# Kernel tuning notes

Hardware: AMD Instinct MI355X
Metric: run time of the kernel (lower is better)

## Reference

```python
import jax, jax.numpy as jnp
import numpy as np

HIDDEN = 1024
B, S = 4, 2048

def setup_inputs() -> dict:
    key = jax.random.key(0)
    k1, k2 = jax.random.split(key)
    hidden_states = jax.random.normal(k1, (B, S, HIDDEN), dtype=jnp.float32)
    # torch nn.Linear weight layout: [out_features, in_features]
    W_proj = jax.random.normal(k2, (3 * HIDDEN, HIDDEN), dtype=jnp.float32) * (1.0 / np.sqrt(HIDDEN))
    b_proj = jnp.zeros((3 * HIDDEN,), dtype=jnp.float32)
    return {"hidden_states": hidden_states, "W_proj": W_proj, "b_proj": b_proj}

def reference(hidden_states, W_proj, b_proj):
    h = hidden_states.shape[-1]
    # fused QKV projection: y = x @ W^T + b
    qkv = jnp.einsum('bsh,oh->bso', hidden_states, W_proj) + b_proj
    q, k, v = jnp.split(qkv, 3, axis=-1)  # each [B,S,H]
    scale = 1.0 / jnp.sqrt(jnp.asarray(h, dtype=q.dtype))
    scores = jnp.einsum('bqh,bkh->bqk', q, k) * scale  # [B,S,S]
    attn = jax.nn.softmax(scores, axis=-1)
    out = jnp.einsum('bqk,bkh->bqh', attn, v)
    return out
```

## Files before the change

kernel.cpp:

```cpp
#include <hip/hip_runtime.h>
#include <stdint.h>

#define HIDDEN 1024
#define BATCH  4
#define SEQ    2048
#define TOKENS (BATCH * SEQ)
#define QKVD   (3 * HIDDEN)

typedef unsigned short u16;
typedef __attribute__((ext_vector_type(8))) short   short8;
typedef __attribute__((ext_vector_type(4))) float   floatx4;

__device__ __forceinline__ u16 f32_bf16_rne(float f) {
    unsigned int u = __float_as_uint(f);
    u += 0x7FFFu + ((u >> 16) & 1u);
    return (u16)(u >> 16);
}

__device__ __forceinline__ void gl16(const u16* g, u16* l) {
    __builtin_amdgcn_global_load_lds(
        (const __attribute__((address_space(1))) void*)g,
        (__attribute__((address_space(3))) void*)l, 16, 0, 0);
}

#define SYNC3() do { __builtin_amdgcn_sched_barrier(0); \
    asm volatile("s_waitcnt vmcnt(3)\n\ts_barrier" ::: "memory"); } while (0)
#define PBAR() do { __builtin_amdgcn_sched_barrier(0); \
    asm volatile("s_barrier" ::: "memory"); } while (0)
#define LG0() asm volatile("s_waitcnt lgkmcnt(0)" ::: "memory")
#define VM4() do { __builtin_amdgcn_sched_barrier(0); \
    asm volatile("s_waitcnt vmcnt(4)" ::: "memory"); } while (0)

__global__ __launch_bounds__(256) void cvt2_bf16_kernel(
        const float* __restrict__ sa, const float* __restrict__ sb,
        u16* __restrict__ da, u16* __restrict__ db, int n4a, int n4tot) {
    int i = blockIdx.x * 256 + threadIdx.x;
    if (i >= n4tot) return;
    float4 v;
    if (i < n4a) v = ((const float4*)sa)[i];
    else         v = ((const float4*)sb)[i - n4a];
    ushort4 o;
    o.x = f32_bf16_rne(v.x); o.y = f32_bf16_rne(v.y);
    o.z = f32_bf16_rne(v.z); o.w = f32_bf16_rne(v.w);
    if (i < n4a) ((ushort4*)da)[i] = o;
    else         ((ushort4*)db)[i - n4a] = o;
}

__global__ __launch_bounds__(512, 2) void gemm_qkv(
        const u16* __restrict__ A, const u16* __restrict__ B,
        u16* __restrict__ C, const float* __restrict__ bias) {
    __shared__ __align__(16) u16 lds[2][2][(128 + 256) * 32];

    const int t    = threadIdx.x;
    const int lane = t & 63;
    const int wid  = t >> 6;
    const int wr   = wid >> 2;
    const int wc   = wid & 3;
    const int bm   = blockIdx.y * 128;
    const int bn   = blockIdx.x * 256;

    const int rA  = t >> 2;
    const int sl  = (t & 3) ^ ((rA >> 1) & 3);
    const u16* gA  = A + (size_t)(bm + rA) * 1024 + sl * 8;
    const u16* gB0 = B + (size_t)(bn + rA) * 1024 + sl * 8;
    const u16* gB1 = gB0 + (size_t)128 * 1024;

    const int fr = lane & 15;
    const int kc = lane >> 4;
    const int fo = ((kc ^ ((fr >> 1) & 3)) << 4);
    const int aoffB = (wr * 64 + fr) * 64 + fo;
    const int boffB = (wc * 64 + fr) * 64 + fo;

    floatx4 acc[4][4];
#pragma unroll
    for (int i = 0; i < 4; i++)
#pragma unroll
        for (int j = 0; j < 4; j++) acc[i][j] = (floatx4){0.f, 0.f, 0.f, 0.f};

    short8 bfr0, bfr1, bfr2, bfr3, va0, va1;

#define LDB4(BASE) \
    bfr0 = *(const short8*)((BASE) + boffB);        \
    bfr1 = *(const short8*)((BASE) + boffB + 1024); \
    bfr2 = *(const short8*)((BASE) + boffB + 2048); \
    bfr3 = *(const short8*)((BASE) + boffB + 3072);

#define MFMA2(MI, A0, A1) \
    __builtin_amdgcn_s_setprio(1); \
    acc[MI][0]     = __builtin_amdgcn_mfma_f32_16x16x32_bf16(A0, bfr0, acc[MI][0], 0, 0, 0); \
    acc[MI][1]     = __builtin_amdgcn_mfma_f32_16x16x32_bf16(A0, bfr1, acc[MI][1], 0, 0, 0); \
    acc[MI][2]     = __builtin_amdgcn_mfma_f32_16x16x32_bf16(A0, bfr2, acc[MI][2], 0, 0, 0); \
    acc[MI][3]     = __builtin_amdgcn_mfma_f32_16x16x32_bf16(A0, bfr3, acc[MI][3], 0, 0, 0); \
    acc[(MI)+1][0] = __builtin_amdgcn_mfma_f32_16x16x32_bf16(A1, bfr0, acc[(MI)+1][0], 0, 0, 0); \
    acc[(MI)+1][1] = __builtin_amdgcn_mfma_f32_16x16x32_bf16(A1, bfr1, acc[(MI)+1][1], 0, 0, 0); \
    acc[(MI)+1][2] = __builtin_amdgcn_mfma_f32_16x16x32_bf16(A1, bfr2, acc[(MI)+1][2], 0, 0, 0); \
    acc[(MI)+1][3] = __builtin_amdgcn_mfma_f32_16x16x32_bf16(A1, bfr3, acc[(MI)+1][3], 0, 0, 0); \
    __builtin_amdgcn_s_setprio(0);

#define ITER(BUF, SBUF, SCOL) { \
    const char* As0_ = (const char*)&lds[BUF][0][0]; \
    const char* Bs0_ = As0_ + 8192; \
    const char* As1_ = (const char*)&lds[BUF][1][0]; \
    const char* Bs1_ = As1_ + 8192; \
    gl16(gA + (SCOL),       (u16*)((char*)&lds[SBUF][0][0]    + wid * 1024)); \
    LDB4(Bs0_); \
    va0 = *(const short8*)(As0_ + aoffB); \
    va1 = *(const short8*)(As0_ + aoffB + 1024); \
    MFMA2(0, va0, va1); \
    gl16(gB0 + (SCOL),      (u16*)((char*)&lds[SBUF][0][4096] + wid * 1024)); \
    gl16(gB1 + (SCOL),      (u16*)((char*)&lds[SBUF][0][8192] + wid * 1024)); \
    va0 = *(const short8*)(As0_ + aoffB + 2048); \
    va1 = *(const short8*)(As0_ + aoffB + 3072); \
    MFMA2(2, va0, va1); \
    SYNC3(); \
    gl16(gA + (SCOL) + 32,  (u16*)((char*)&lds[SBUF][1][0]    + wid * 1024)); \
    LDB4(Bs1_); \
    va0 = *(const short8*)(As1_ + aoffB); \
    va1 = *(const short8*)(As1_ + aoffB + 1024); \
    MFMA2(0, va0, va1); \
    gl16(gB0 + (SCOL) + 32, (u16*)((char*)&lds[SBUF][1][4096] + wid * 1024)); \
    gl16(gB1 + (SCOL) + 32, (u16*)((char*)&lds[SBUF][1][8192] + wid * 1024)); \
    va0 = *(const short8*)(As1_ + aoffB + 2048); \
    va1 = *(const short8*)(As1_ + aoffB + 3072); \
    MFMA2(2, va0, va1); \
    SYNC3(); }

    gl16(gA,       (u16*)((char*)&lds[0][0][0]    + wid * 1024));
    gl16(gB0,      (u16*)((char*)&lds[0][0][4096] + wid * 1024));
    gl16(gB1,      (u16*)((char*)&lds[0][0][8192] + wid * 1024));
    gl16(gA + 32,  (u16*)((char*)&lds[0][1][0]    + wid * 1024));
    gl16(gB0 + 32, (u16*)((char*)&lds[0][1][4096] + wid * 1024));
    gl16(gB1 + 32, (u16*)((char*)&lds[0][1][8192] + wid * 1024));
    SYNC3();

    const int nk = 1024 >> 6;
    for (int kt = 0; kt < nk; kt += 2) {
        const int c1 = (kt + 1) << 6;
        const int c2 = (kt + 2 < nk ? (kt + 2) : (nk - 1)) << 6;
        ITER(0, 1, c1)
        ITER(1, 0, c2)
    }
    asm volatile("s_waitcnt vmcnt(0)" ::: "memory");

#undef ITER
#undef MFMA2
#undef LDB4

    const int crow0 = bm + wr * 64 + kc * 4;
    const int ccol0 = bn + wc * 64 + fr;
    float bv[4];
#pragma unroll
    for (int ni = 0; ni < 4; ni++) bv[ni] = bias[ccol0 + ni * 16];
#pragma unroll
    for (int mi = 0; mi < 4; mi++)
#pragma unroll
        for (int ni = 0; ni < 4; ni++)
#pragma unroll
            for (int r = 0; r < 4; r++)
                C[(size_t)(crow0 + mi * 16 + r) * QKVD + (ccol0 + ni * 16)] =
                    f32_bf16_rne(acc[mi][ni][r] + bv[ni]);
}

template <int EPI, int WM>
__global__ __launch_bounds__(512, 2) void gemm_bt(
        const u16* __restrict__ A, const u16* __restrict__ B,
        void* __restrict__ Cv, const float* __restrict__ bias,
        int K, int lda, int ldb, int ldc,
        size_t sA, size_t sB, size_t sC, float scale) {
    constexpr int BM    = 2 * WM;
    constexpr int MIH   = WM / 32;
    constexpr int ASLAB = BM * 64;
    constexpr int BSLAB = 256 * 64;
    constexpr int BUFB  = 2 * ASLAB + 2 * BSLAB;
    __shared__ __align__(16) char lds[2][BUFB];

    const int t    = threadIdx.x;
    const int lane = t & 63;
    const int wid  = t >> 6;
    const int wr   = wid >> 2;
    const int wc   = wid & 3;
    const int bm   = blockIdx.y * BM;
    const int bn   = blockIdx.x * 256;

    const u16* Ab = A + (size_t)blockIdx.z * sA;
    const u16* Bb = B + (size_t)blockIdx.z * sB;

    const int r0 = t >> 2;
    const int sl = (t & 3) ^ ((r0 >> 1) & 3);
    const u16* gA0 = Ab + (size_t)(bm + r0) * lda + sl * 8;
    const u16* gA1 = gA0 + (size_t)128 * lda;
    const u16* gB0 = Bb + (size_t)(bn + r0) * ldb + sl * 8;
    const u16* gB1 = gB0 + (size_t)128 * ldb;

    const int fr  = lane & 15;
    const int kc  = lane >> 4;
    const int frb = fr * 64 + ((kc ^ ((fr >> 1) & 3)) << 4);

    floatx4 acc[2 * MIH][4];
#pragma unroll
    for (int i = 0; i < 2 * MIH; i++)
#pragma unroll
        for (int j = 0; j < 4; j++) acc[i][j] = (floatx4){0.f, 0.f, 0.f, 0.f};

    short8 aF[MIH][2], bLo[2][2], bHi[2][2];

    auto rdA = [&](short8 (&dst)[MIH][2], const char* bp, int miBase) {
#pragma unroll
        for (int m = 0; m < MIH; m++)
#pragma unroll
            for (int ks = 0; ks < 2; ks++)
                dst[m][ks] = *(const short8*)(bp + ks * ASLAB +
                    (wr * WM + (miBase + m) * 16) * 64 + frb);
    };
    auto rdB = [&](short8 (&dst)[2][2], const char* bp, int niBase) {
#pragma unroll
        for (int n = 0; n < 2; n++)
#pragma unroll
            for (int ks = 0; ks < 2; ks++)
                dst[n][ks] = *(const short8*)(bp + 2 * ASLAB + ks * BSLAB +
                    (wc * 64 + (niBase + n) * 16) * 64 + frb);
    };
    auto mf = [&](short8 (&av)[MIH][2], short8 (&bv)[2][2], int miB, int niB) {
        __builtin_amdgcn_s_setprio(1);
#pragma unroll
        for (int m = 0; m < MIH; m++)
#pragma unroll
            for (int n = 0; n < 2; n++)
#pragma unroll
                for (int ks = 0; ks < 2; ks++)
                    acc[miB + m][niB + n] = __builtin_amdgcn_mfma_f32_16x16x32_bf16(
                        av[m][ks], bv[n][ks], acc[miB + m][niB + n], 0, 0, 0);
        __builtin_amdgcn_s_setprio(0);
    };

#define STA(buf, ks, sc) do { \
    char* d = &lds[buf][(ks) * ASLAB] + wid * 1024; \
    gl16(gA0 + (sc) + (ks) * 32, (u16*)d); \
    if constexpr (WM == 128) gl16(gA1 + (sc) + (ks) * 32, (u16*)(d + 8192)); \
  } while (0)
#define STB(buf, ks, sc) do { \
    char* d = &lds[buf][2 * ASLAB + (ks) * BSLAB] + wid * 1024; \
    gl16(gB0 + (sc) + (ks) * 32, (u16*)d); \
    gl16(gB1 + (sc) + (ks) * 32, (u16*)(d + 8192)); \
  } while (0)

#define GROUP(q, S1, S2, S3, S4) { \
    const char* bp = &lds[q][0]; \
    rdA(aF, bp, 0); rdB(bLo, bp, 0); S1; PBAR(); LG0(); \
    mf(aF, bLo, 0, 0);   PBAR(); \
    rdB(bHi, bp, 2);                S2; PBAR(); LG0(); \
    mf(aF, bHi, 0, 2);   PBAR(); \
    rdA(aF, bp, MIH);               S3; PBAR(); LG0(); \
    mf(aF, bHi, MIH, 2); PBAR(); \
    S4; VM4(); PBAR(); \
    mf(aF, bLo, MIH, 0); PBAR(); \
}

    STA(0, 0, 0); STA(0, 1, 0); STB(0, 0, 0); STB(0, 1, 0);
    STB(1, 0, 64); STB(1, 1, 64);
    VM4(); PBAR();

    const int nk = K >> 6;
    for (int T = 0; T < nk; T += 2) {
        const int c1 = (T + 1) << 6;
        const int c2 = (T + 2 < nk ? T + 2 : nk - 1) << 6;
        const int c3 = (T + 3 < nk ? T + 3 : nk - 1) << 6;
        GROUP(0, STA(1, 0, c1), STA(1, 1, c1), STB(0, 0, c2), STB(0, 1, c2))
        GROUP(1, STA(0, 0, c2), STA(0, 1, c2), STB(1, 0, c3), STB(1, 1, c3))
    }
    asm volatile("s_waitcnt vmcnt(0)" ::: "memory");

#undef GROUP
#undef STB
#undef STA

    const int crow0 = bm + wr * WM + kc * 4;
    const int ccol0 = bn + wc * 64 + fr;
    const size_t coff = (size_t)blockIdx.z * sC;

    float* C = (float*)Cv;
#pragma unroll
    for (int mi = 0; mi < 2 * MIH; mi++)
#pragma unroll
        for (int ni = 0; ni < 4; ni++)
#pragma unroll
            for (int r = 0; r < 4; r++) {
                float v = acc[mi][ni][r];
                if (EPI == 1) v *= scale;
                C[coff + (size_t)(crow0 + mi * 16 + r) * ldc + (ccol0 + ni * 16)] = v;
            }
}

__global__ __launch_bounds__(256) void softmax_tr_kernel(
        const float* __restrict__ S, u16* __restrict__ P,
        const u16* __restrict__ qkv, u16* __restrict__ Vt) {
    __shared__ float redm[4];
    __shared__ float reds[4];
    __shared__ u16 tile[64][66];
    const int t = threadIdx.x;

    if ((int)blockIdx.x < TOKENS) {
        const size_t base = (size_t)blockIdx.x * SEQ;
        const int lane = t & 63, wid = t >> 6;
        const float4* src = (const float4*)(S + base);
        float4 a = src[t], b = src[t + 256];

        float m = fmaxf(fmaxf(fmaxf(a.x, a.y), fmaxf(a.z, a.w)),
                        fmaxf(fmaxf(b.x, b.y), fmaxf(b.z, b.w)));
#pragma unroll
        for (int off = 32; off; off >>= 1) m = fmaxf(m, __shfl_xor(m, off, 64));
        if (lane == 0) redm[wid] = m;
        __syncthreads();
        m = fmaxf(fmaxf(redm[0], redm[1]), fmaxf(redm[2], redm[3]));

        float e[8];
        e[0] = __expf(a.x - m); e[1] = __expf(a.y - m);
        e[2] = __expf(a.z - m); e[3] = __expf(a.w - m);
        e[4] = __expf(b.x - m); e[5] = __expf(b.y - m);
        e[6] = __expf(b.z - m); e[7] = __expf(b.w - m);
        float s = e[0] + e[1] + e[2] + e[3] + e[4] + e[5] + e[6] + e[7];
#pragma unroll
        for (int off = 32; off; off >>= 1) s += __shfl_xor(s, off, 64);
        if (lane == 0) reds[wid] = s;
        __syncthreads();
        s = reds[0] + reds[1] + reds[2] + reds[3];
        const float r = 1.f / s;

        ushort4* dst = (ushort4*)(P + base);
        ushort4 o0, o1;
        o0.x = f32_bf16_rne(e[0] * r); o0.y = f32_bf16_rne(e[1] * r);
        o0.z = f32_bf16_rne(e[2] * r); o0.w = f32_bf16_rne(e[3] * r);
        o1.x = f32_bf16_rne(e[4] * r); o1.y = f32_bf16_rne(e[5] * r);
        o1.z = f32_bf16_rne(e[6] * r); o1.w = f32_bf16_rne(e[7] * r);
        dst[t] = o0;
        dst[t + 256] = o1;
    } else {
        const int bx = blockIdx.x - TOKENS;
        const int b  = bx >> 9;
        const int s0 = (bx & 31) * 64;
        const int h0 = ((bx >> 5) & 15) * 64;
        const int c = t & 63, r4 = t >> 6;
#pragma unroll
        for (int i = 0; i < 16; i++) {
            int sl = i * 4 + r4;
            tile[sl][c] = qkv[(size_t)(b * SEQ + s0 + sl) * QKVD + 2 * HIDDEN + h0 + c];
        }
        __syncthreads();
#pragma unroll
        for (int i = 0; i < 16; i++) {
            int hl = i * 4 + r4;
            Vt[(size_t)(b * HIDDEN + h0 + hl) * SEQ + s0 + c] = tile[c][hl];
        }
    }
}

extern "C" void kernel_launch(void* const* d_in, const int* in_sizes, int n_in,
                              void* d_out, int out_size, void* d_ws, size_t ws_size,
                              hipStream_t stream) {
    const float* x    = (const float*)d_in[0];
    const float* W    = (const float*)d_in[1];
    const float* bias = (const float*)d_in[2];
    float* out = (float*)d_out;

    u16* Xb  = (u16*)d_ws;
    u16* Wb  = Xb + (size_t)TOKENS * HIDDEN;
    u16* qkv = Wb + (size_t)QKVD * HIDDEN;
    float* scores = (float*)(qkv + (size_t)TOKENS * QKVD);
    u16* P  = (u16*)(scores + (size_t)BATCH * SEQ * SEQ);
    u16* Vt = P + (size_t)BATCH * SEQ * SEQ;

    {
        const int n4a = TOKENS * HIDDEN / 4;
        const int n4b = QKVD * HIDDEN / 4;
        const int n4t = n4a + n4b;
        cvt2_bf16_kernel<<<(n4t + 255) / 256, 256, 0, stream>>>(x, W, Xb, Wb, n4a, n4t);
    }

    gemm_qkv<<<dim3(QKVD / 256, TOKENS / 128, 1), 512, 0, stream>>>(
        Xb, Wb, qkv, bias);

    gemm_bt<1, 128><<<dim3(SEQ / 256, SEQ / 256, BATCH), 512, 0, stream>>>(
        qkv, qkv + HIDDEN, scores, nullptr, HIDDEN, QKVD, QKVD, SEQ,
        (size_t)SEQ * QKVD, (size_t)SEQ * QKVD, (size_t)SEQ * SEQ, 0.03125f);

    softmax_tr_kernel<<<TOKENS + 2048, 256, 0, stream>>>(scores, P, qkv, Vt);

    gemm_bt<2, 64><<<dim3(HIDDEN / 256, SEQ / 128, BATCH), 512, 0, stream>>>(
        P, Vt, out, nullptr, SEQ, SEQ, SEQ, HIDDEN,
        (size_t)SEQ * SEQ, (size_t)HIDDEN * SEQ, (size_t)SEQ * HIDDEN, 1.f);
}
```

Measured before the change: 253.0 us.

## Shrink QKV GEMM block tile to 128x128 with 4 waves

Changes the QKV projection GEMM from a 128x256 tile with 8 waves to a 128x128 tile with 4 waves, doubling the grid along N. Staging is reworked so each thread issues two A and two B async loads per k-chunk, and the wait count is updated to match. The aim is more blocks for better CU load balance and smaller LDS per block, which may allow more resident blocks. The cost is less operand reuse per block and more global/L2 traffic for the A matrix.

```diff
diff --git a/kernel.cpp b/kernel.cpp
--- a/kernel.cpp
+++ b/kernel.cpp
@@ -23,8 +23,8 @@
         (__attribute__((address_space(3))) void*)l, 16, 0, 0);
 }
 
-#define SYNC3() do { __builtin_amdgcn_sched_barrier(0); \
-    asm volatile("s_waitcnt vmcnt(3)\n\ts_barrier" ::: "memory"); } while (0)
+#define SYNC4() do { __builtin_amdgcn_sched_barrier(0); \
+    asm volatile("s_waitcnt vmcnt(4)\n\ts_barrier" ::: "memory"); } while (0)
 #define PBAR() do { __builtin_amdgcn_sched_barrier(0); \
     asm volatile("s_barrier" ::: "memory"); } while (0)
 #define LG0() asm volatile("s_waitcnt lgkmcnt(0)" ::: "memory")
@@ -46,30 +46,31 @@
     else         ((ushort4*)db)[i - n4a] = o;
 }
 
-__global__ __launch_bounds__(512, 2) void gemm_qkv(
+__global__ __launch_bounds__(256, 2) void gemm_qkv(
         const u16* __restrict__ A, const u16* __restrict__ B,
         u16* __restrict__ C, const float* __restrict__ bias) {
-    __shared__ __align__(16) u16 lds[2][2][(128 + 256) * 32];
+    __shared__ __align__(16) u16 lds[2][2][(128 + 128) * 32];
 
     const int t    = threadIdx.x;
     const int lane = t & 63;
     const int wid  = t >> 6;
-    const int wr   = wid >> 2;
-    const int wc   = wid & 3;
+    const int wm   = (wid >> 1) * 64;
+    const int wn   = (wid & 1) * 64;
     const int bm   = blockIdx.y * 128;
-    const int bn   = blockIdx.x * 256;
-
-    const int rA  = t >> 2;
-    const int sl  = (t & 3) ^ ((rA >> 1) & 3);
-    const u16* gA  = A + (size_t)(bm + rA) * 1024 + sl * 8;
-    const u16* gB0 = B + (size_t)(bn + rA) * 1024 + sl * 8;
-    const u16* gB1 = gB0 + (size_t)128 * 1024;
+    const int bn   = blockIdx.x * 128;
+
+    const int r0 = t >> 2;
+    const int sl = (t & 3) ^ ((r0 >> 1) & 3);
+    const u16* gA0 = A + (size_t)(bm + r0) * 1024 + sl * 8;
+    const u16* gA1 = gA0 + (size_t)64 * 1024;
+    const u16* gB0 = B + (size_t)(bn + r0) * 1024 + sl * 8;
+    const u16* gB1 = gB0 + (size_t)64 * 1024;
 
     const int fr = lane & 15;
     const int kc = lane >> 4;
     const int fo = ((kc ^ ((fr >> 1) & 3)) << 4);
-    const int aoffB = (wr * 64 + fr) * 64 + fo;
-    const int boffB = (wc * 64 + fr) * 64 + fo;
+    const int aoffB = (wm + fr) * 64 + fo;
+    const int boffB = 8192 + (wn + fr) * 64 + fo;
 
     floatx4 acc[4][4];
 #pragma unroll
@@ -97,41 +98,46 @@
     acc[(MI)+1][3] = __builtin_amdgcn_mfma_f32_16x16x32_bf16(A1, bfr3, acc[(MI)+1][3], 0, 0, 0); \
     __builtin_amdgcn_s_setprio(0);
 
+#define STG_A(CH, SC) do { char* d_ = (char*)(CH); \
+    gl16(gA0 + (SC), (u16*)(d_ + wid * 1024)); \
+    gl16(gA1 + (SC), (u16*)(d_ + 4096 + wid * 1024)); } while (0)
+#define STG_B(CH, SC) do { char* d_ = (char*)(CH) + 8192; \
+    gl16(gB0 + (SC), (u16*)(d_ + wid * 1024)); \
+    gl16(gB1 + (SC), (u16*)(d_ + 4096 + wid * 1024)); } while (0)
+
 #define ITER(BUF, SBUF, SCOL) { \
-    const char* As0_ = (const char*)&lds[BUF][0][0]; \
-    const char* Bs0_ = As0_ + 8192; \
-    const char* As1_ = (const char*)&lds[BUF][1][0]; \
-    const char* Bs1_ = As1_ + 8192; \
-    gl16(gA + (SCOL),       (u16*)((char*)&lds[SBUF][0][0]    + wid * 1024)); \
-    LDB4(Bs0_); \
-    va0 = *(const short8*)(As0_ + aoffB); \
-    va1 = *(const short8*)(As0_ + aoffB + 1024); \
+    const char* k0 = (const char*)&lds[BUF][0][0]; \
+    const char* k1 = (const char*)&lds[BUF][1][0]; \
+    char* s0 = (char*)&lds[SBUF][0][0]; \
+    char* s1 = (char*)&lds[SBUF][1][0]; \
+     \
+    STG_A(s0, SCOL); \
+    LDB4(k0); \
+    va0 = *(const short8*)(k0 + aoffB); \
+    va1 = *(const short8*)(k0 + aoffB + 1024); \
     MFMA2(0, va0, va1); \
-    gl16(gB0 + (SCOL),      (u16*)((char*)&lds[SBUF][0][4096] + wid * 1024)); \
-    gl16(gB1 + (SCOL),      (u16*)((char*)&lds[SBUF][0][8192] + wid * 1024)); \
-    va0 = *(const short8*)(As0_ + aoffB + 2048); \
-    va1 = *(const short8*)(As0_ + aoffB + 3072); \
+     \
+    STG_B(s0, SCOL); \
+    va0 = *(const short8*)(k0 + aoffB + 2048); \
+    va1 = *(const short8*)(k0 + aoffB + 3072); \
     MFMA2(2, va0, va1); \
-    SYNC3(); \
-    gl16(gA + (SCOL) + 32,  (u16*)((char*)&lds[SBUF][1][0]    + wid * 1024)); \
-    LDB4(Bs1_); \
-    va0 = *(const short8*)(As1_ + aoffB); \
-    va1 = *(const short8*)(As1_ + aoffB + 1024); \
+    SYNC4(); \
+     \
+    STG_A(s1, (SCOL) + 32); \
+    LDB4(k1); \
+    va0 = *(const short8*)(k1 + aoffB); \
+    va1 = *(const short8*)(k1 + aoffB + 1024); \
     MFMA2(0, va0, va1); \
-    gl16(gB0 + (SCOL) + 32, (u16*)((char*)&lds[SBUF][1][4096] + wid * 1024)); \
-    gl16(gB1 + (SCOL) + 32, (u16*)((char*)&lds[SBUF][1][8192] + wid * 1024)); \
-    va0 = *(const short8*)(As1_ + aoffB + 2048); \
-    va1 = *(const short8*)(As1_ + aoffB + 3072); \
+     \
+    STG_B(s1, (SCOL) + 32); \
+    va0 = *(const short8*)(k1 + aoffB + 2048); \
+    va1 = *(const short8*)(k1 + aoffB + 3072); \
     MFMA2(2, va0, va1); \
-    SYNC3(); }
-
-    gl16(gA,       (u16*)((char*)&lds[0][0][0]    + wid * 1024));
-    gl16(gB0,      (u16*)((char*)&lds[0][0][4096] + wid * 1024));
-    gl16(gB1,      (u16*)((char*)&lds[0][0][8192] + wid * 1024));
-    gl16(gA + 32,  (u16*)((char*)&lds[0][1][0]    + wid * 1024));
-    gl16(gB0 + 32, (u16*)((char*)&lds[0][1][4096] + wid * 1024));
-    gl16(gB1 + 32, (u16*)((char*)&lds[0][1][8192] + wid * 1024));
-    SYNC3();
+    SYNC4(); }
+
+    STG_A(&lds[0][0][0], 0); STG_B(&lds[0][0][0], 0);
+    STG_A(&lds[0][1][0], 32); STG_B(&lds[0][1][0], 32);
+    SYNC4();
 
     const int nk = 1024 >> 6;
     for (int kt = 0; kt < nk; kt += 2) {
@@ -143,11 +149,13 @@
     asm volatile("s_waitcnt vmcnt(0)" ::: "memory");
 
 #undef ITER
+#undef STG_B
+#undef STG_A
 #undef MFMA2
 #undef LDB4
 
-    const int crow0 = bm + wr * 64 + kc * 4;
-    const int ccol0 = bn + wc * 64 + fr;
+    const int crow0 = bm + wm + kc * 4;
+    const int ccol0 = bn + wn + fr;
     float bv[4];
 #pragma unroll
     for (int ni = 0; ni < 4; ni++) bv[ni] = bias[ccol0 + ni * 16];
@@ -376,7 +384,7 @@
         cvt2_bf16_kernel<<<(n4t + 255) / 256, 256, 0, stream>>>(x, W, Xb, Wb, n4a, n4t);
     }
 
-    gemm_qkv<<<dim3(QKVD / 256, TOKENS / 128, 1), 512, 0, stream>>>(
+    gemm_qkv<<<dim3(QKVD / 128, TOKENS / 128, 1), 256, 0, stream>>>(
         Xb, Wb, qkv, bias);
 
     gemm_bt<1, 128><<<dim3(SEQ / 256, SEQ / 256, BATCH), 512, 0, stream>>>(
```

Result: no change. 255.0 us (+0.8%).
